# Optimization experiments

Measured on AMD Instinct MI355X. Metric: run time of the kernel, lower is better.

Reference implementation:

```python
import jax, jax.numpy as jnp
import numpy as np

NUM_VARS = 10000
NUM_CLAUSES = 100000
K = 3  # literals per clause (3-SAT)
BATCH = 256


def setup_inputs() -> dict:
    key = jax.random.key(0)
    k1, k2, k3 = jax.random.split(key, 3)
    # fuzzy truth assignments in [0,1): [num_vars, batch]
    input = jax.random.uniform(k1, (NUM_VARS, BATCH), dtype=jnp.float32)
    # clause-literal incidence: variable index and negation flag per slot
    lit_idx = jax.random.randint(k2, (NUM_CLAUSES, K), 0, NUM_VARS, dtype=jnp.int64)
    lit_neg = jax.random.randint(k3, (NUM_CLAUSES, K), 0, 2, dtype=jnp.int64)
    return {"input": input, "lit_idx": lit_idx, "lit_neg": lit_neg}


def reference(input, lit_idx, lit_neg):
    # Gather literal values per clause slot: [num_clauses, K, batch]
    vals = input[lit_idx]
    # Goedel negation for negated literals: x -> 1 - x
    vals = jnp.where((lit_neg == 1)[:, :, None], 1.0 - vals, vals)
    # Fuzzy disjunction (Goedel = max) within each clause: [num_clauses, batch]
    clause_vals = jnp.max(vals, axis=1)
    # Fuzzy conjunction (Goedel = min) across clauses: [batch]
    return jnp.min(clause_vals, axis=0)
```

## Files before the change

kernel.cpp:

```cpp
#include <hip/hip_runtime.h>
#include <hip/hip_fp16.h>

#define NUM_VARS    10000
#define NUM_CLAUSES 100000
#define BATCH       256
#define CPI         8
#define NCHUNK      (NUM_CLAUSES / CPI)
#define WAVES_H     4096

typedef __attribute__((ext_vector_type(4))) _Float16 half4_t;
typedef __attribute__((ext_vector_type(2))) _Float16 half2_t;
typedef __attribute__((ext_vector_type(4))) float    float4_t;

static __device__ __forceinline__ half2_t h2max(half2_t a, half2_t b) {
    half2_t r;
    r.x = (a.x > b.x) ? a.x : b.x;
    r.y = (a.y > b.y) ? a.y : b.y;
    return r;
}
static __device__ __forceinline__ half2_t h2min(half2_t a, half2_t b) {
    half2_t r;
    r.x = (a.x < b.x) ? a.x : b.x;
    r.y = (a.y < b.y) ? a.y : b.y;
    return r;
}

__global__ __launch_bounds__(256) void fuzzy_convert_init(
    const float4_t* __restrict__ in,
    half4_t*        __restrict__ out16,
    float*          __restrict__ out)
{
    if (blockIdx.x == 0 && threadIdx.x < BATCH)
        out[threadIdx.x] = __uint_as_float(0x7F800000u);

    const int n4 = NUM_VARS * BATCH / 4;
    for (int i = blockIdx.x * blockDim.x + threadIdx.x; i < n4;
         i += gridDim.x * blockDim.x) {
        float4_t v = in[i];
        half4_t h;
        h.x = (_Float16)v.x;  h.y = (_Float16)v.y;
        h.z = (_Float16)v.z;  h.w = (_Float16)v.w;
        out16[i] = h;
    }
}

__global__ __launch_bounds__(512, 8) void fuzzy_cnf_fp16(
    const half2_t* __restrict__ input16,
    const int*     __restrict__ lit_idx,
    const int*     __restrict__ lit_neg,
    float*         __restrict__ out)
{
    const int wave   = threadIdx.x >> 6;
    const int lane   = threadIdx.x & 63;
    const int xcd    = blockIdx.x & 7;
    const int half   = (xcd >= 4) ? 1 : 0;
    const int hBlock = ((blockIdx.x >> 3) << 2) | (xcd & 3);
    const int gwave  = __builtin_amdgcn_readfirstlane(hBlock * 8 + wave);
    const int coff   = half * 64 + lane;

    half2_t acc;
    acc.x = (_Float16)30000.0f;  acc.y = (_Float16)30000.0f;

    #pragma unroll 1
    for (int ch = gwave; ch < NCHUNK; ch += WAVES_H) {
        const int base = ch * (CPI * 3);

        int idx[CPI * 3];
        int neg[CPI * 3];
        #pragma unroll
        for (int j = 0; j < CPI * 3; ++j) idx[j] = lit_idx[base + j];
        #pragma unroll
        for (int j = 0; j < CPI * 3; ++j) neg[j] = lit_neg[base + j];

        half2_t x[CPI * 3];
        #pragma unroll
        for (int j = 0; j < CPI * 3; ++j)
            x[j] = input16[idx[j] * 128 + coff];

        #pragma unroll
        for (int q = 0; q < CPI; ++q) {
            half2_t v[3];
            #pragma unroll
            for (int l = 0; l < 3; ++l) {
                const int j = 3 * q + l;
                const _Float16 s = neg[j] ? (_Float16)-1.0f : (_Float16)1.0f;
                const _Float16 n = neg[j] ? (_Float16)1.0f  : (_Float16)0.0f;
                half2_t sv; sv.x = s; sv.y = s;
                half2_t nv; nv.x = n; nv.y = n;
                v[l] = x[j] * sv + nv;
            }
            acc = h2min(acc, h2max(h2max(v[0], v[1]), v[2]));
        }
    }

    __shared__ float sm[8][128];
    sm[wave][lane * 2 + 0] = (float)acc.x;
    sm[wave][lane * 2 + 1] = (float)acc.y;
    __syncthreads();

    const int t = threadIdx.x;
    if (t < 128) {
        float m = sm[0][t];
        #pragma unroll
        for (int w = 1; w < 8; ++w) m = fminf(m, sm[w][t]);
        atomicMin((unsigned int*)out + half * 128 + t, __float_as_uint(m));
    }
}

extern "C" void kernel_launch(void* const* d_in, const int* in_sizes, int n_in,
                              void* d_out, int out_size, void* d_ws, size_t ws_size,
                              hipStream_t stream) {
    const float* input   = (const float*)d_in[0];
    const int*   lit_idx = (const int*)d_in[1];
    const int*   lit_neg = (const int*)d_in[2];
    float*       out     = (float*)d_out;

    half4_t* input16 = (half4_t*)d_ws;

    fuzzy_convert_init<<<1024, 256, 0, stream>>>((const float4_t*)input,
                                                 input16, out);
    fuzzy_cnf_fp16<<<1024, 512, 0, stream>>>((const half2_t*)input16,
                                             lit_idx, lit_neg, out);
}
```

Before: 79.36 us.

## Software-pipeline clause gathers with double-buffered banks and a fully unrolled chunk loop

Replaces the runtime chunk loop with a fully unrolled, double-buffered schedule. Each step issues the gathers for the current chunk before computing the previous one, and prefetches the next chunk's index and negation metadata. Chunk size drops to 4 clauses and the grid is halved to 512 blocks of 512 threads, with a fixed 12 unrolled iterations plus one tail chunk. The aim is to hide gather latency inside each wave instead of depending on high occupancy. The cost is more registers, with launch bounds relaxed to 4 blocks per unit, and fewer waves in flight.

```diff
diff --git a/kernel.cpp b/kernel.cpp
--- a/kernel.cpp
+++ b/kernel.cpp
@@ -4,9 +4,10 @@
 #define NUM_VARS    10000
 #define NUM_CLAUSES 100000
 #define BATCH       256
-#define CPI         8
+#define CPI         4
 #define NCHUNK      (NUM_CLAUSES / CPI)
-#define WAVES_H     4096
+#define WAVES_H     2048
+#define UNROLL_CH   12
 
 typedef __attribute__((ext_vector_type(4))) _Float16 half4_t;
 typedef __attribute__((ext_vector_type(2))) _Float16 half2_t;
@@ -23,6 +24,44 @@
     r.x = (a.x < b.x) ? a.x : b.x;
     r.y = (a.y < b.y) ? a.y : b.y;
     return r;
+}
+static __device__ __forceinline__ half2_t litval(half2_t x, int neg) {
+    const _Float16 s = neg ? (_Float16)-1.0f : (_Float16)1.0f;
+    const _Float16 n = neg ? (_Float16)1.0f  : (_Float16)0.0f;
+    half2_t sv; sv.x = s; sv.y = s;
+    half2_t nv; nv.x = n; nv.y = n;
+    return x * sv + nv;
+}
+
+struct Bank {
+    int     idx[CPI * 3];
+    int     neg[CPI * 3];
+    half2_t g  [CPI * 3];
+};
+
+static __device__ __forceinline__ void loadMeta(Bank& b,
+        const int* __restrict__ lit_idx, const int* __restrict__ lit_neg,
+        int ch) {
+    const int base = ch * (CPI * 3);
+    #pragma unroll
+    for (int j = 0; j < CPI * 3; ++j) b.idx[j] = lit_idx[base + j];
+    #pragma unroll
+    for (int j = 0; j < CPI * 3; ++j) b.neg[j] = lit_neg[base + j];
+}
+static __device__ __forceinline__ void issueG(Bank& b,
+        const half2_t* __restrict__ in, int coff) {
+    #pragma unroll
+    for (int j = 0; j < CPI * 3; ++j)
+        b.g[j] = in[(b.idx[j] << 7) + coff];
+}
+static __device__ __forceinline__ void computeC(Bank& b, half2_t& acc) {
+    #pragma unroll
+    for (int q = 0; q < CPI; ++q) {
+        const half2_t v0 = litval(b.g[3*q+0], b.neg[3*q+0]);
+        const half2_t v1 = litval(b.g[3*q+1], b.neg[3*q+1]);
+        const half2_t v2 = litval(b.g[3*q+2], b.neg[3*q+2]);
+        acc = h2min(acc, h2max(h2max(v0, v1), v2));
+    }
 }
 
 __global__ __launch_bounds__(256) void fuzzy_convert_init(
@@ -44,7 +83,7 @@
     }
 }
 
-__global__ __launch_bounds__(512, 8) void fuzzy_cnf_fp16(
+__global__ __launch_bounds__(512, 4) void fuzzy_cnf_fp16(
     const half2_t* __restrict__ input16,
     const int*     __restrict__ lit_idx,
     const int*     __restrict__ lit_neg,
@@ -61,36 +100,28 @@
     half2_t acc;
     acc.x = (_Float16)30000.0f;  acc.y = (_Float16)30000.0f;
 
-    #pragma unroll 1
-    for (int ch = gwave; ch < NCHUNK; ch += WAVES_H) {
-        const int base = ch * (CPI * 3);
+    Bank A, B;
+    const int c = gwave;
 
-        int idx[CPI * 3];
-        int neg[CPI * 3];
-        #pragma unroll
-        for (int j = 0; j < CPI * 3; ++j) idx[j] = lit_idx[base + j];
-        #pragma unroll
-        for (int j = 0; j < CPI * 3; ++j) neg[j] = lit_neg[base + j];
+    loadMeta(A, lit_idx, lit_neg, c);
+    issueG(A, input16, coff);
+    loadMeta(B, lit_idx, lit_neg, c + WAVES_H);
 
-        half2_t x[CPI * 3];
-        #pragma unroll
-        for (int j = 0; j < CPI * 3; ++j)
-            x[j] = input16[idx[j] * 128 + coff];
+    #pragma unroll
+    for (int k = 1; k < UNROLL_CH; ++k) {
+        Bank& cur = (k & 1) ? B : A;
+        Bank& prv = (k & 1) ? A : B;
+        issueG(cur, input16, coff);
+        computeC(prv, acc);
+        if (k + 1 < UNROLL_CH)
+            loadMeta(prv, lit_idx, lit_neg, c + (k + 1) * WAVES_H);
+    }
+    computeC((UNROLL_CH - 1) & 1 ? B : A, acc);
 
-        #pragma unroll
-        for (int q = 0; q < CPI; ++q) {
-            half2_t v[3];
-            #pragma unroll
-            for (int l = 0; l < 3; ++l) {
-                const int j = 3 * q + l;
-                const _Float16 s = neg[j] ? (_Float16)-1.0f : (_Float16)1.0f;
-                const _Float16 n = neg[j] ? (_Float16)1.0f  : (_Float16)0.0f;
-                half2_t sv; sv.x = s; sv.y = s;
-                half2_t nv; nv.x = n; nv.y = n;
-                v[l] = x[j] * sv + nv;
-            }
-            acc = h2min(acc, h2max(h2max(v[0], v[1]), v[2]));
-        }
+    if (c + UNROLL_CH * WAVES_H < NCHUNK) {
+        loadMeta(A, lit_idx, lit_neg, c + UNROLL_CH * WAVES_H);
+        issueG(A, input16, coff);
+        computeC(A, acc);
     }
 
     __shared__ float sm[8][128];
@@ -119,6 +150,6 @@
 
     fuzzy_convert_init<<<1024, 256, 0, stream>>>((const float4_t*)input,
                                                  input16, out);
-    fuzzy_cnf_fp16<<<1024, 512, 0, stream>>>((const half2_t*)input16,
-                                             lit_idx, lit_neg, out);
+    fuzzy_cnf_fp16<<<512, 512, 0, stream>>>((const half2_t*)input16,
+                                            lit_idx, lit_neg, out);
 }
```

Result: slower. 83.60 us (+5.3%).

## Stage packed clause metadata in LDS and double-buffer gathers per wave

Applied to the files above, without the earlier changes.

Each block now cooperatively loads a contiguous slab of 200 clauses, packs each literal's index and negation flag into a single int, and stores them in shared memory. Each wave then processes 25 fixed clauses, using two register banks so that the gathers for the next group are issued before the current group is computed. The grid becomes exactly 1000 blocks with a static split of the work. This is meant to remove redundant scattered global metadata loads and hide gather latency. In exchange it costs higher register use, lower occupancy bounds, and an extra block-level barrier.

```diff
diff --git a/kernel.cpp b/kernel.cpp
--- a/kernel.cpp
+++ b/kernel.cpp
@@ -4,13 +4,16 @@
 #define NUM_VARS    10000
 #define NUM_CLAUSES 100000
 #define BATCH       256
-#define CPI         8
-#define NCHUNK      (NUM_CLAUSES / CPI)
-#define WAVES_H     4096
+#define SLAB        200
+#define CPW         25
+#define CPI         4
+#define NCH         6
+#define LDS_W       76
 
 typedef __attribute__((ext_vector_type(4))) _Float16 half4_t;
 typedef __attribute__((ext_vector_type(2))) _Float16 half2_t;
 typedef __attribute__((ext_vector_type(4))) float    float4_t;
+typedef __attribute__((ext_vector_type(4))) int      int4_t;
 
 static __device__ __forceinline__ half2_t h2max(half2_t a, half2_t b) {
     half2_t r;
@@ -23,6 +26,41 @@
     r.x = (a.x < b.x) ? a.x : b.x;
     r.y = (a.y < b.y) ? a.y : b.y;
     return r;
+}
+
+struct Bank { int pk[12]; half2_t g[12]; };
+
+static __device__ __forceinline__ void ldsMeta(Bank& b, const int* wl, int intOff) {
+    const int4_t* p = (const int4_t*)(wl + intOff);
+    const int4_t a = p[0], c = p[1], d = p[2];
+    b.pk[0]=a.x; b.pk[1]=a.y; b.pk[2]=a.z;  b.pk[3]=a.w;
+    b.pk[4]=c.x; b.pk[5]=c.y; b.pk[6]=c.z;  b.pk[7]=c.w;
+    b.pk[8]=d.x; b.pk[9]=d.y; b.pk[10]=d.z; b.pk[11]=d.w;
+}
+
+static __device__ __forceinline__ void issueG(Bank& b, const char* inB, int coffB) {
+    #pragma unroll
+    for (int j = 0; j < 12; ++j) {
+        const unsigned vb = ((unsigned)(b.pk[j] & ~1) << 8) + coffB;
+        b.g[j] = *(const half2_t*)(inB + vb);
+    }
+}
+
+static __device__ __forceinline__ void computeC(const Bank& b, half2_t& acc,
+        half2_t one2, half2_t mone2, half2_t zero2) {
+    #pragma unroll
+    for (int q = 0; q < CPI; ++q) {
+        half2_t v[3];
+        #pragma unroll
+        for (int l = 0; l < 3; ++l) {
+            const int j = 3 * q + l;
+            const bool neg = b.pk[j] & 1;
+            const half2_t sv = neg ? mone2 : one2;
+            const half2_t nv = neg ? one2  : zero2;
+            v[l] = b.g[j] * sv + nv;
+        }
+        acc = h2min(acc, h2max(h2max(v[0], v[1]), v[2]));
+    }
 }
 
 __global__ __launch_bounds__(256) void fuzzy_convert_init(
@@ -44,56 +82,76 @@
     }
 }
 
-__global__ __launch_bounds__(512, 8) void fuzzy_cnf_fp16(
+__global__ __launch_bounds__(512, 6) void fuzzy_cnf_fp16(
     const half2_t* __restrict__ input16,
     const int*     __restrict__ lit_idx,
     const int*     __restrict__ lit_neg,
     float*         __restrict__ out)
 {
+    __shared__ __align__(16) int lds_pk[8 * LDS_W];
+    __shared__ float sm[8][128];
+
     const int wave   = threadIdx.x >> 6;
     const int lane   = threadIdx.x & 63;
     const int xcd    = blockIdx.x & 7;
     const int half   = (xcd >= 4) ? 1 : 0;
     const int hBlock = ((blockIdx.x >> 3) << 2) | (xcd & 3);
-    const int gwave  = __builtin_amdgcn_readfirstlane(hBlock * 8 + wave);
-    const int coff   = half * 64 + lane;
+    const int coffB  = (half * 64 + lane) * 4;
+
+    const int base = hBlock * (SLAB * 3);
+    for (int t = threadIdx.x; t < SLAB * 3; t += 512) {
+        const int c  = t / 3;
+        const int r  = t - c * 3;
+        const int w  = c / CPW;
+        const int lc = c - w * CPW;
+        lds_pk[w * LDS_W + lc * 3 + r] = (lit_idx[base + t] << 1) | lit_neg[base + t];
+    }
+    __syncthreads();
+
+    const int*  wl  = lds_pk + wave * LDS_W;
+    const char* inB = (const char*)input16;
+
+    half2_t one2, mone2, zero2;
+    one2.x  = (_Float16) 1.0f;  one2.y  = (_Float16) 1.0f;
+    mone2.x = (_Float16)-1.0f;  mone2.y = (_Float16)-1.0f;
+    zero2.x = (_Float16) 0.0f;  zero2.y = (_Float16) 0.0f;
 
     half2_t acc;
     acc.x = (_Float16)30000.0f;  acc.y = (_Float16)30000.0f;
 
-    #pragma unroll 1
-    for (int ch = gwave; ch < NCHUNK; ch += WAVES_H) {
-        const int base = ch * (CPI * 3);
+    Bank A, B;
+    ldsMeta(A, wl, 0);  issueG(A, inB, coffB);
+    ldsMeta(B, wl, 12); issueG(B, inB, coffB);
 
-        int idx[CPI * 3];
-        int neg[CPI * 3];
+    #pragma unroll
+    for (int k = 0; k < NCH - 2; ++k) {
+        Bank& done = (k & 1) ? B : A;
+        computeC(done, acc, one2, mone2, zero2);
+        ldsMeta(done, wl, (k + 2) * 12);
+        issueG(done, inB, coffB);
+    }
+    computeC(A, acc, one2, mone2, zero2);
+    computeC(B, acc, one2, mone2, zero2);
+
+    {
+        Bank T;
+        T.pk[0] = wl[72]; T.pk[1] = wl[73]; T.pk[2] = wl[74];
         #pragma unroll
-        for (int j = 0; j < CPI * 3; ++j) idx[j] = lit_idx[base + j];
+        for (int j = 0; j < 3; ++j) {
+            const unsigned vb = ((unsigned)(T.pk[j] & ~1) << 8) + coffB;
+            T.g[j] = *(const half2_t*)(inB + vb);
+        }
+        half2_t v[3];
         #pragma unroll
-        for (int j = 0; j < CPI * 3; ++j) neg[j] = lit_neg[base + j];
-
-        half2_t x[CPI * 3];
-        #pragma unroll
-        for (int j = 0; j < CPI * 3; ++j)
-            x[j] = input16[idx[j] * 128 + coff];
-
-        #pragma unroll
-        for (int q = 0; q < CPI; ++q) {
-            half2_t v[3];
-            #pragma unroll
-            for (int l = 0; l < 3; ++l) {
-                const int j = 3 * q + l;
-                const _Float16 s = neg[j] ? (_Float16)-1.0f : (_Float16)1.0f;
-                const _Float16 n = neg[j] ? (_Float16)1.0f  : (_Float16)0.0f;
-                half2_t sv; sv.x = s; sv.y = s;
-                half2_t nv; nv.x = n; nv.y = n;
-                v[l] = x[j] * sv + nv;
-            }
-            acc = h2min(acc, h2max(h2max(v[0], v[1]), v[2]));
+        for (int l = 0; l < 3; ++l) {
+            const bool neg = T.pk[l] & 1;
+            const half2_t sv = neg ? mone2 : one2;
+            const half2_t nv = neg ? one2  : zero2;
+            v[l] = T.g[l] * sv + nv;
         }
+        acc = h2min(acc, h2max(h2max(v[0], v[1]), v[2]));
     }
 
-    __shared__ float sm[8][128];
     sm[wave][lane * 2 + 0] = (float)acc.x;
     sm[wave][lane * 2 + 1] = (float)acc.y;
     __syncthreads();
@@ -119,6 +177,6 @@
 
     fuzzy_convert_init<<<1024, 256, 0, stream>>>((const float4_t*)input,
                                                  input16, out);
-    fuzzy_cnf_fp16<<<1024, 512, 0, stream>>>((const half2_t*)input16,
+    fuzzy_cnf_fp16<<<1000, 512, 0, stream>>>((const half2_t*)input16,
                                              lit_idx, lit_neg, out);
 }
```

Result: slower. 81.67 us (+2.9%).
